# Kernel optimization log

Measured on AMD Instinct MI355X. Metric: run time of the kernel, lower is better.

The kernel has to match this reference:

```python
import jax, jax.numpy as jnp
import numpy as np

DIM = 1024
HEADS = 16
DIM_HEAD = 64
INNER = HEADS * DIM_HEAD  # 1024
P = INNER  # num_param_tokens
B, N = 4, 2048
LN_EPS = 1e-5
NORM_EPS = 1e-12


def _pattention(x, key_tok, val_tok):
    # x: [..., dim_in]; key_tok: [P, dim_in]; val_tok: [P, dim_out]
    scale = key_tok.shape[1] ** (-0.5)
    sim = jnp.einsum('bnd,pd->bnp', x, key_tok) * scale
    # F.normalize(p=2, dim=-1) with eps=1e-12
    nrm = jnp.maximum(jnp.linalg.norm(sim, axis=-1, keepdims=True), NORM_EPS)
    attn = jax.nn.gelu(sim / nrm, approximate=False)  # torch F.gelu default = exact erf
    return jnp.einsum('bnp,pe->bne', attn, val_tok)


def setup_inputs() -> dict:
    key = jax.random.key(0)
    ks = jax.random.split(key, 11)
    d = {
        'x': jax.random.normal(ks[0], (B, N, DIM), dtype=jnp.float32),
        'ln_gamma': jnp.ones((DIM,), dtype=jnp.float32),
        'ln_beta': jnp.zeros((DIM,), dtype=jnp.float32),
        'q_key': jax.random.normal(ks[1], (P, DIM), dtype=jnp.float32),
        'q_val': jax.random.normal(ks[2], (P, INNER), dtype=jnp.float32),
        'k_key': jax.random.normal(ks[3], (P, DIM), dtype=jnp.float32),
        'k_val': jax.random.normal(ks[4], (P, INNER), dtype=jnp.float32),
        'v_key': jax.random.normal(ks[5], (P, DIM), dtype=jnp.float32),
        'v_val': jax.random.normal(ks[6], (P, INNER), dtype=jnp.float32),
        'o_key': jax.random.normal(ks[7], (P, INNER), dtype=jnp.float32),
        'o_val': jax.random.normal(ks[8], (P, DIM), dtype=jnp.float32),
    }
    return d


def reference(x, ln_gamma, ln_beta, q_key, q_val, k_key, k_val, v_key, v_val, o_key, o_val):
    # LayerNorm (torch default: elementwise affine, eps=1e-5)
    mu = jnp.mean(x, axis=-1, keepdims=True)
    var = jnp.mean(jnp.square(x - mu), axis=-1, keepdims=True)
    x_norm = (x - mu) / jnp.sqrt(var + LN_EPS) * ln_gamma + ln_beta

    q = _pattention(x_norm, q_key, q_val)  # [B, N, INNER]
    k = _pattention(x_norm, k_key, k_val)
    v = _pattention(x_norm, v_key, v_val)

    # b n (h d) -> b h n d
    def split_heads(t):
        return t.reshape(B, N, HEADS, DIM_HEAD).transpose(0, 2, 1, 3)

    q, k, v = split_heads(q), split_heads(k), split_heads(v)
    scale = DIM_HEAD ** (-0.5)
    dots = jnp.einsum('bhnd,bhmd->bhnm', q, k) * scale  # [B, H, N, N]
    attn = jax.nn.softmax(dots, axis=-1)  # dropout p=0 -> identity
    out = jnp.einsum('bhnm,bhmd->bhnd', attn, v)
    out = out.transpose(0, 2, 1, 3).reshape(B, N, INNER)  # b h n d -> b n (h d)
    return _pattention(out, o_key, o_val)
```

## Files before the change

### kernel.cpp

```cpp
#include <hip/hip_runtime.h>
#include <hip/hip_bf16.h>
#include <stdint.h>

#define DIMSZ 1024
#define BN_TOT 8192
#define NSEQ 2048
#define NHEADS 16
#define DHEAD 64

typedef __attribute__((ext_vector_type(8))) __bf16 bf16x8;
typedef __attribute__((ext_vector_type(4))) float f32x4;

__device__ __forceinline__ float bf2f(ushort u) {
  return __uint_as_float(((uint32_t)u) << 16);
}
__device__ __forceinline__ ushort f2bf(float f) {
  uint32_t u = __float_as_uint(f);
  u += 0x7FFFu + ((u >> 16) & 1u);
  return (ushort)(u >> 16);
}
__device__ __forceinline__ uint32_t cvt_pk_bf16(float lo, float hi) {
  uint32_t r;
  asm("v_cvt_pk_bf16_f32 %0, %1, %2" : "=v"(r) : "v"(lo), "v"(hi));
  return r;
}

__global__ __launch_bounds__(256) void layernorm_k(
    const float* __restrict__ x, const float* __restrict__ gamma,
    const float* __restrict__ beta, ushort* __restrict__ xn) {
  const int row = blockIdx.x;
  const int tid = threadIdx.x;
  const float* xr = x + (size_t)row * DIMSZ;
  float4 v = *(const float4*)(xr + tid * 4);
  float s = v.x + v.y + v.z + v.w;
  float ss = v.x * v.x + v.y * v.y + v.z * v.z + v.w * v.w;
#pragma unroll
  for (int o = 1; o < 64; o <<= 1) { s += __shfl_xor(s, o); ss += __shfl_xor(ss, o); }
  __shared__ float red[2][4];
  const int wid = tid >> 6;
  if ((tid & 63) == 0) { red[0][wid] = s; red[1][wid] = ss; }
  __syncthreads();
  s = red[0][0] + red[0][1] + red[0][2] + red[0][3];
  ss = red[1][0] + red[1][1] + red[1][2] + red[1][3];
  const float mu = s * (1.0f / DIMSZ);
  const float var = ss * (1.0f / DIMSZ) - mu * mu;
  const float rstd = rsqrtf(var + 1e-5f);
  float4 g = *(const float4*)(gamma + tid * 4);
  float4 bb = *(const float4*)(beta + tid * 4);
  ushort4 o4;
  o4.x = f2bf((v.x - mu) * rstd * g.x + bb.x);
  o4.y = f2bf((v.y - mu) * rstd * g.y + bb.y);
  o4.z = f2bf((v.z - mu) * rstd * g.z + bb.z);
  o4.w = f2bf((v.w - mu) * rstd * g.w + bb.w);
  *(ushort4*)(xn + (size_t)row * DIMSZ + tid * 4) = o4;
}

__global__ __launch_bounds__(256) void normgelu_k(
    const float* __restrict__ sim, ushort* __restrict__ out) {
  const int row = blockIdx.x;
  const int tid = threadIdx.x;
  const float* sr = sim + (size_t)row * DIMSZ;
  float4 v = *(const float4*)(sr + tid * 4);
  float ss = v.x * v.x + v.y * v.y + v.z * v.z + v.w * v.w;
#pragma unroll
  for (int o = 1; o < 64; o <<= 1) ss += __shfl_xor(ss, o);
  __shared__ float red[4];
  if ((tid & 63) == 0) red[tid >> 6] = ss;
  __syncthreads();
  ss = red[0] + red[1] + red[2] + red[3];
  const float inv = 1.0f / fmaxf(sqrtf(ss), 1e-12f);
  ushort4 o4;
  float x0;
  x0 = v.x * inv; o4.x = f2bf(0.5f * x0 * (1.0f + erff(x0 * 0.70710678118654752f)));
  x0 = v.y * inv; o4.y = f2bf(0.5f * x0 * (1.0f + erff(x0 * 0.70710678118654752f)));
  x0 = v.z * inv; o4.z = f2bf(0.5f * x0 * (1.0f + erff(x0 * 0.70710678118654752f)));
  x0 = v.w * inv; o4.w = f2bf(0.5f * x0 * (1.0f + erff(x0 * 0.70710678118654752f)));
  *(ushort4*)(out + (size_t)row * DIMSZ + tid * 4) = o4;
}

__global__ void cvt_k(const float* __restrict__ in, ushort* __restrict__ out, int n) {
  int i = (blockIdx.x * 256 + threadIdx.x) * 4;
  if (i < n) {
    float4 v = *(const float4*)(in + i);
    ushort4 o;
    o.x = f2bf(v.x); o.y = f2bf(v.y); o.z = f2bf(v.z); o.w = f2bf(v.w);
    *(ushort4*)(out + i) = o;
  }
}

__global__ __launch_bounds__(256) void transpose_cvt_k(
    const float* __restrict__ in, ushort* __restrict__ out) {
  __shared__ float t[32][33];
  const int tx = threadIdx.x & 31;
  const int ty = threadIdx.x >> 5;
  const int bx = blockIdx.x * 32;
  const int by = blockIdx.y * 32;
#pragma unroll
  for (int i = 0; i < 32; i += 8)
    t[ty + i][tx] = in[(size_t)(by + ty + i) * DIMSZ + bx + tx];
  __syncthreads();
#pragma unroll
  for (int i = 0; i < 32; i += 8)
    out[(size_t)(bx + ty + i) * DIMSZ + by + tx] = f2bf(t[tx][ty + i]);
}

__global__ __launch_bounds__(256) void transpose_v_k(
    const ushort* __restrict__ vb, ushort* __restrict__ vt) {
  __shared__ ushort t[32][33];
  const int bh = blockIdx.x;
  const int nt = blockIdx.y;
  const int dt = blockIdx.z;
  const int b = bh >> 4, h = bh & 15;
  const int tx = threadIdx.x & 31;
  const int ty = threadIdx.x >> 5;
  const size_t inbase = ((size_t)b * NSEQ + nt * 32) * DIMSZ + h * DHEAD + dt * 32;
#pragma unroll
  for (int i = 0; i < 32; i += 8)
    t[ty + i][tx] = vb[inbase + (size_t)(ty + i) * DIMSZ + tx];
  __syncthreads();
  const size_t outbase = ((size_t)bh * DHEAD + dt * 32) * NSEQ + nt * 32;
#pragma unroll
  for (int i = 0; i < 32; i += 8)
    vt[outbase + (size_t)(ty + i) * NSEQ + tx] = t[tx][ty + i];
}

template <int OUT_BF16>
__global__ __launch_bounds__(256) void gemm_nt_k(
    const ushort* __restrict__ A, const ushort* __restrict__ B,
    void* __restrict__ Cout, int M, int N, int K) {
  __shared__ ushort As[128 * 40];
  __shared__ ushort Bs[128 * 40];
  const int tid = threadIdx.x;
  const int lane = tid & 63;
  const int wid = tid >> 6;
  const int i0 = blockIdx.x * 128;
  const int n0 = blockIdx.y * 128;
  const int wr = (wid >> 1) * 64;
  const int wc = (wid & 1) * 64;
  f32x4 acc[4][4];
#pragma unroll
  for (int m = 0; m < 4; ++m)
#pragma unroll
    for (int n = 0; n < 4; ++n) acc[m][n] = (f32x4){0.f, 0.f, 0.f, 0.f};
  const int srow = tid >> 2;
  const int skc = (tid & 3) * 8;
  const ushort* Ag = A + (size_t)i0 * K + skc;
  const ushort* Bg = B + (size_t)n0 * K + skc;
  const int fr = lane & 15;
  const int kg = (lane >> 4) * 8;
  uint4 a0 = *(const uint4*)(Ag + (size_t)srow * K);
  uint4 a1 = *(const uint4*)(Ag + (size_t)(srow + 64) * K);
  uint4 b0 = *(const uint4*)(Bg + (size_t)srow * K);
  uint4 b1 = *(const uint4*)(Bg + (size_t)(srow + 64) * K);
  for (int k0 = 0; k0 < K; k0 += 32) {
    __syncthreads();
    *(uint4*)&As[srow * 40 + skc] = a0;
    *(uint4*)&As[(srow + 64) * 40 + skc] = a1;
    *(uint4*)&Bs[srow * 40 + skc] = b0;
    *(uint4*)&Bs[(srow + 64) * 40 + skc] = b1;
    __syncthreads();
    if (k0 + 32 < K) {
      a0 = *(const uint4*)(Ag + (size_t)srow * K + k0 + 32);
      a1 = *(const uint4*)(Ag + (size_t)(srow + 64) * K + k0 + 32);
      b0 = *(const uint4*)(Bg + (size_t)srow * K + k0 + 32);
      b1 = *(const uint4*)(Bg + (size_t)(srow + 64) * K + k0 + 32);
    }
    bf16x8 af[4], bfr[4];
#pragma unroll
    for (int m = 0; m < 4; ++m)
      af[m] = *(const bf16x8*)&As[(wr + m * 16 + fr) * 40 + kg];
#pragma unroll
    for (int n = 0; n < 4; ++n)
      bfr[n] = *(const bf16x8*)&Bs[(wc + n * 16 + fr) * 40 + kg];
#pragma unroll
    for (int m = 0; m < 4; ++m)
#pragma unroll
      for (int n = 0; n < 4; ++n)
        acc[m][n] = __builtin_amdgcn_mfma_f32_16x16x32_bf16(af[m], bfr[n], acc[m][n], 0, 0, 0);
  }
  const int rq = lane >> 4;
#pragma unroll
  for (int m = 0; m < 4; ++m) {
#pragma unroll
    for (int n = 0; n < 4; ++n) {
#pragma unroll
      for (int rr = 0; rr < 4; ++rr) {
        const int row = i0 + wr + m * 16 + rq * 4 + rr;
        const int col = n0 + wc + n * 16 + fr;
        if (OUT_BF16)
          ((ushort*)Cout)[(size_t)row * N + col] = f2bf(acc[m][n][rr]);
        else
          ((float*)Cout)[(size_t)row * N + col] = acc[m][n][rr];
      }
    }
  }
}

__global__ __launch_bounds__(256) void flash_mfma_k(
    const ushort* __restrict__ Qm, const ushort* __restrict__ Km,
    const ushort* __restrict__ Vt, ushort* __restrict__ Om) {
  __shared__ ushort Ks[64 * 72];
  __shared__ ushort Vs[64 * 72];
  __shared__ ushort Ps[4][32 * 72];
  const int tid = threadIdx.x;
  const int lane = tid & 63;
  const int wid = tid >> 6;
  const int bh = blockIdx.x;
  const int qb = blockIdx.y;
  const int bidx = bh >> 4;
  const int h = bh & 15;
  const size_t rowbase = (size_t)bidx * NSEQ;
  const int colbase = h * DHEAD;
  const int fr = lane & 15;
  const int g = lane >> 4;
  const int kg = g * 8;
  const int q0 = qb * 128 + wid * 32;

  bf16x8 qf[2][2];
#pragma unroll
  for (int m = 0; m < 2; ++m)
#pragma unroll
    for (int ks = 0; ks < 2; ++ks)
      qf[m][ks] = *(const bf16x8*)(Qm + (rowbase + q0 + m * 16 + fr) * (size_t)DIMSZ +
                                   colbase + ks * 32 + kg);

  f32x4 oaccT[2][4];
#pragma unroll
  for (int m = 0; m < 2; ++m)
#pragma unroll
    for (int n = 0; n < 4; ++n) oaccT[m][n] = (f32x4){0.f, 0.f, 0.f, 0.f};
  float m2[2] = {-1e30f, -1e30f};
  float l_run[2] = {0.f, 0.f};
  const float c1 = 0.125f * 1.44269504088896340736f;

  const ushort* Kg = Km + rowbase * DIMSZ + colbase;
  const ushort* Vg = Vt + (size_t)bh * DHEAD * NSEQ;
  const int sr = tid >> 3;
  const int c8 = (tid & 7) * 8;

  uint4 k0 = *(const uint4*)(Kg + (size_t)sr * DIMSZ + c8);
  uint4 k1 = *(const uint4*)(Kg + (size_t)(sr + 32) * DIMSZ + c8);
  uint4 v0 = *(const uint4*)(Vg + (size_t)sr * NSEQ + c8);
  uint4 v1 = *(const uint4*)(Vg + (size_t)(sr + 32) * NSEQ + c8);

  for (int kt = 0; kt < NSEQ / 64; ++kt) {
    __syncthreads();
    *(uint4*)&Ks[sr * 72 + c8] = k0;
    *(uint4*)&Ks[(sr + 32) * 72 + c8] = k1;
    *(uint4*)&Vs[sr * 72 + c8] = v0;
    *(uint4*)&Vs[(sr + 32) * 72 + c8] = v1;
    __syncthreads();
    if (kt + 1 < NSEQ / 64) {
      k0 = *(const uint4*)(Kg + (size_t)((kt + 1) * 64 + sr) * DIMSZ + c8);
      k1 = *(const uint4*)(Kg + (size_t)((kt + 1) * 64 + sr + 32) * DIMSZ + c8);
      v0 = *(const uint4*)(Vg + (size_t)sr * NSEQ + (kt + 1) * 64 + c8);
      v1 = *(const uint4*)(Vg + (size_t)(sr + 32) * NSEQ + (kt + 1) * 64 + c8);
    }

    f32x4 s[2][4];
#pragma unroll
    for (int m = 0; m < 2; ++m)
#pragma unroll
      for (int n = 0; n < 4; ++n) s[m][n] = (f32x4){0.f, 0.f, 0.f, 0.f};
    __builtin_amdgcn_s_setprio(1);
#pragma unroll
    for (int ks = 0; ks < 2; ++ks) {
      bf16x8 ak[4];
#pragma unroll
      for (int n = 0; n < 4; ++n)
        ak[n] = *(const bf16x8*)&Ks[(n * 16 + fr) * 72 + ks * 32 + kg];
#pragma unroll
      for (int m = 0; m < 2; ++m)
#pragma unroll
        for (int n = 0; n < 4; ++n)
          s[m][n] = __builtin_amdgcn_mfma_f32_16x16x32_bf16(ak[n], qf[m][ks], s[m][n], 0, 0, 0);
    }
    __builtin_amdgcn_s_setprio(0);

#pragma unroll
    for (int m = 0; m < 2; ++m) {
      float tm = fmaxf(fmaxf(fmaxf(s[m][0][0], s[m][0][1]), fmaxf(s[m][0][2], s[m][0][3])),
                       fmaxf(fmaxf(s[m][1][0], s[m][1][1]), fmaxf(s[m][1][2], s[m][1][3])));
      tm = fmaxf(tm,
                 fmaxf(fmaxf(fmaxf(s[m][2][0], s[m][2][1]), fmaxf(s[m][2][2], s[m][2][3])),
                       fmaxf(fmaxf(s[m][3][0], s[m][3][1]), fmaxf(s[m][3][2], s[m][3][3]))));
      tm = fmaxf(tm, __shfl_xor(tm, 16));
      tm = fmaxf(tm, __shfl_xor(tm, 32));
      const float mn2 = fmaxf(m2[m], tm * c1);
      const float al = exp2f(m2[m] - mn2);
      float ps = 0.f;
#pragma unroll
      for (int n = 0; n < 4; ++n)
#pragma unroll
        for (int rr = 0; rr < 4; ++rr) {
          const float p = exp2f(fmaf(s[m][n][rr], c1, -mn2));
          s[m][n][rr] = p;
          ps += p;
        }
      ps += __shfl_xor(ps, 16);
      ps += __shfl_xor(ps, 32);
      l_run[m] = l_run[m] * al + ps;
      m2[m] = mn2;
#pragma unroll
      for (int n = 0; n < 4; ++n) oaccT[m][n] *= al;
    }

    ushort* pw = &Ps[wid][0];
#pragma unroll
    for (int m = 0; m < 2; ++m)
#pragma unroll
      for (int n = 0; n < 4; ++n) {
        uint2 w;
        w.x = cvt_pk_bf16(s[m][n][0], s[m][n][1]);
        w.y = cvt_pk_bf16(s[m][n][2], s[m][n][3]);
        *(uint2*)&pw[(m * 16 + fr) * 72 + n * 16 + g * 4] = w;
      }

    __builtin_amdgcn_s_setprio(1);
#pragma unroll
    for (int ks = 0; ks < 2; ++ks) {
      bf16x8 av[4], pb[2];
#pragma unroll
      for (int nd = 0; nd < 4; ++nd)
        av[nd] = *(const bf16x8*)&Vs[(nd * 16 + fr) * 72 + ks * 32 + kg];
#pragma unroll
      for (int m = 0; m < 2; ++m)
        pb[m] = *(const bf16x8*)&Ps[wid][(m * 16 + fr) * 72 + ks * 32 + kg];
#pragma unroll
      for (int m = 0; m < 2; ++m)
#pragma unroll
        for (int nd = 0; nd < 4; ++nd)
          oaccT[m][nd] = __builtin_amdgcn_mfma_f32_16x16x32_bf16(av[nd], pb[m], oaccT[m][nd], 0, 0, 0);
    }
    __builtin_amdgcn_s_setprio(0);
  }

#pragma unroll
  for (int m = 0; m < 2; ++m) {
    const float invl = 1.0f / l_run[m];
    const size_t row = rowbase + q0 + m * 16 + fr;
#pragma unroll
    for (int nd = 0; nd < 4; ++nd) {
      uint2 w;
      w.x = cvt_pk_bf16(oaccT[m][nd][0] * invl, oaccT[m][nd][1] * invl);
      w.y = cvt_pk_bf16(oaccT[m][nd][2] * invl, oaccT[m][nd][3] * invl);
      *(uint2*)(Om + row * DIMSZ + colbase + nd * 16 + g * 4) = w;
    }
  }
}

extern "C" void kernel_launch(void* const* d_in, const int* in_sizes, int n_in,
                              void* d_out, int out_size, void* d_ws, size_t ws_size,
                              hipStream_t stream) {
  (void)in_sizes; (void)n_in; (void)out_size; (void)ws_size;
  const float* x     = (const float*)d_in[0];
  const float* ln_g  = (const float*)d_in[1];
  const float* ln_b  = (const float*)d_in[2];
  const float* q_key = (const float*)d_in[3];
  const float* q_val = (const float*)d_in[4];
  const float* k_key = (const float*)d_in[5];
  const float* k_val = (const float*)d_in[6];
  const float* v_key = (const float*)d_in[7];
  const float* v_val = (const float*)d_in[8];
  const float* o_key = (const float*)d_in[9];
  const float* o_val = (const float*)d_in[10];
  float* out = (float*)d_out;

  char* ws = (char*)d_ws;
  const size_t MB = 1024 * 1024;
  ushort* xn    = (ushort*)(ws + 0 * MB);
  ushort* wkey  = (ushort*)(ws + 16 * MB);
  ushort* wvalT = (ushort*)(ws + 24 * MB);
  ushort* gelu  = (ushort*)(ws + 32 * MB);
  ushort* qb    = (ushort*)(ws + 48 * MB);
  ushort* kb    = (ushort*)(ws + 64 * MB);
  ushort* vb    = (ushort*)(ws + 80 * MB);
  ushort* aout  = (ushort*)(ws + 96 * MB);
  ushort* vt    = gelu;
  float* sim = (float*)d_out;

  const int NW = DIMSZ * DIMSZ;

  layernorm_k<<<BN_TOT, 256, 0, stream>>>(x, ln_g, ln_b, xn);
  cvt_k<<<1024, 256, 0, stream>>>(q_key, wkey + 0 * (size_t)NW, NW);
  cvt_k<<<1024, 256, 0, stream>>>(k_key, wkey + 1 * (size_t)NW, NW);
  cvt_k<<<1024, 256, 0, stream>>>(v_key, wkey + 2 * (size_t)NW, NW);
  cvt_k<<<1024, 256, 0, stream>>>(o_key, wkey + 3 * (size_t)NW, NW);
  dim3 tg(32, 32);
  transpose_cvt_k<<<tg, 256, 0, stream>>>(q_val, wvalT + 0 * (size_t)NW);
  transpose_cvt_k<<<tg, 256, 0, stream>>>(k_val, wvalT + 1 * (size_t)NW);
  transpose_cvt_k<<<tg, 256, 0, stream>>>(v_val, wvalT + 2 * (size_t)NW);
  transpose_cvt_k<<<tg, 256, 0, stream>>>(o_val, wvalT + 3 * (size_t)NW);

  dim3 gg(BN_TOT / 128, DIMSZ / 128);
  ushort* outs[3] = {qb, kb, vb};
  for (int t = 0; t < 3; ++t) {
    gemm_nt_k<0><<<gg, 256, 0, stream>>>(xn, wkey + t * (size_t)NW, sim, BN_TOT, DIMSZ, DIMSZ);
    normgelu_k<<<BN_TOT, 256, 0, stream>>>(sim, gelu);
    gemm_nt_k<1><<<gg, 256, 0, stream>>>(gelu, wvalT + t * (size_t)NW, outs[t], BN_TOT, DIMSZ, DIMSZ);
  }
  transpose_v_k<<<dim3(64, 64, 2), 256, 0, stream>>>(vb, vt);
  flash_mfma_k<<<dim3(64, 16), 256, 0, stream>>>(qb, kb, vt, aout);
  gemm_nt_k<0><<<gg, 256, 0, stream>>>(aout, wkey + 3 * (size_t)NW, sim, BN_TOT, DIMSZ, DIMSZ);
  normgelu_k<<<BN_TOT, 256, 0, stream>>>(sim, gelu);
  gemm_nt_k<0><<<gg, 256, 0, stream>>>(gelu, wvalT + 3 * (size_t)NW, (void*)out, BN_TOT, DIMSZ, DIMSZ);
}
```

Measured before the change: 451.1 us.

## Use direct global-to-LDS loads in GEMM, lazy softmax rescale, occupancy hint

The GEMM now loads tiles with global_load_lds straight into unpadded LDS, replacing the register-staged prefetch. This drops VGPR staging but loses the overlap of the next tile's load with compute and can add bank conflicts because the padding is gone. The flash-attention kernel gets a launch-bounds occupancy hint of 4 blocks. Its online softmax now rescales the running max only when the new max exceeds the old one by more than 8 in log2 units, and sums the row with a tree reduction. This skips many rescale multiplies and exps at the cost of some extra numeric range.

New measurement: 452.4 us. No clear change (+0.3%).

```diff
diff --git a/kernel.cpp b/kernel.cpp
--- a/kernel.cpp
+++ b/kernel.cpp
@@ -23,6 +23,11 @@
   uint32_t r;
   asm("v_cvt_pk_bf16_f32 %0, %1, %2" : "=v"(r) : "v"(lo), "v"(hi));
   return r;
+}
+__device__ __forceinline__ void gl_lds16(const ushort* g, ushort* l) {
+  __builtin_amdgcn_global_load_lds(
+      (const __attribute__((address_space(1))) void*)g,
+      (__attribute__((address_space(3))) void*)l, 16, 0, 0);
 }
 
 __global__ __launch_bounds__(256) void layernorm_k(
@@ -128,8 +133,8 @@
 __global__ __launch_bounds__(256) void gemm_nt_k(
     const ushort* __restrict__ A, const ushort* __restrict__ B,
     void* __restrict__ Cout, int M, int N, int K) {
-  __shared__ ushort As[128 * 40];
-  __shared__ ushort Bs[128 * 40];
+  __shared__ ushort As[128 * 32];
+  __shared__ ushort Bs[128 * 32];
   const int tid = threadIdx.x;
   const int lane = tid & 63;
   const int wid = tid >> 6;
@@ -142,36 +147,28 @@
   for (int m = 0; m < 4; ++m)
 #pragma unroll
     for (int n = 0; n < 4; ++n) acc[m][n] = (f32x4){0.f, 0.f, 0.f, 0.f};
-  const int srow = tid >> 2;
-  const int skc = (tid & 3) * 8;
-  const ushort* Ag = A + (size_t)i0 * K + skc;
-  const ushort* Bg = B + (size_t)n0 * K + skc;
   const int fr = lane & 15;
   const int kg = (lane >> 4) * 8;
-  uint4 a0 = *(const uint4*)(Ag + (size_t)srow * K);
-  uint4 a1 = *(const uint4*)(Ag + (size_t)(srow + 64) * K);
-  uint4 b0 = *(const uint4*)(Bg + (size_t)srow * K);
-  uint4 b1 = *(const uint4*)(Bg + (size_t)(srow + 64) * K);
+  const int srow = wid * 32 + (lane >> 2);
+  const int skc = (lane & 3) * 8;
+  const ushort* Ag = A + (size_t)(i0 + srow) * K + skc;
+  const ushort* Bg = B + (size_t)(n0 + srow) * K + skc;
+  ushort* AsW = As + wid * 1024;
+  ushort* BsW = Bs + wid * 1024;
   for (int k0 = 0; k0 < K; k0 += 32) {
     __syncthreads();
-    *(uint4*)&As[srow * 40 + skc] = a0;
-    *(uint4*)&As[(srow + 64) * 40 + skc] = a1;
-    *(uint4*)&Bs[srow * 40 + skc] = b0;
-    *(uint4*)&Bs[(srow + 64) * 40 + skc] = b1;
+    gl_lds16(Ag + k0, AsW);
+    gl_lds16(Ag + (size_t)16 * K + k0, AsW + 512);
+    gl_lds16(Bg + k0, BsW);
+    gl_lds16(Bg + (size_t)16 * K + k0, BsW + 512);
     __syncthreads();
-    if (k0 + 32 < K) {
-      a0 = *(const uint4*)(Ag + (size_t)srow * K + k0 + 32);
-      a1 = *(const uint4*)(Ag + (size_t)(srow + 64) * K + k0 + 32);
-      b0 = *(const uint4*)(Bg + (size_t)srow * K + k0 + 32);
-      b1 = *(const uint4*)(Bg + (size_t)(srow + 64) * K + k0 + 32);
-    }
     bf16x8 af[4], bfr[4];
 #pragma unroll
     for (int m = 0; m < 4; ++m)
-      af[m] = *(const bf16x8*)&As[(wr + m * 16 + fr) * 40 + kg];
+      af[m] = *(const bf16x8*)&As[(wr + m * 16 + fr) * 32 + kg];
 #pragma unroll
     for (int n = 0; n < 4; ++n)
-      bfr[n] = *(const bf16x8*)&Bs[(wc + n * 16 + fr) * 40 + kg];
+      bfr[n] = *(const bf16x8*)&Bs[(wc + n * 16 + fr) * 32 + kg];
 #pragma unroll
     for (int m = 0; m < 4; ++m)
 #pragma unroll
@@ -196,7 +193,7 @@
   }
 }
 
-__global__ __launch_bounds__(256) void flash_mfma_k(
+__global__ __launch_bounds__(256, 4) void flash_mfma_k(
     const ushort* __restrict__ Qm, const ushort* __restrict__ Km,
     const ushort* __restrict__ Vt, ushort* __restrict__ Om) {
   __shared__ ushort Ks[64 * 72];
@@ -286,23 +283,32 @@
                        fmaxf(fmaxf(s[m][3][0], s[m][3][1]), fmaxf(s[m][3][2], s[m][3][3]))));
       tm = fmaxf(tm, __shfl_xor(tm, 16));
       tm = fmaxf(tm, __shfl_xor(tm, 32));
-      const float mn2 = fmaxf(m2[m], tm * c1);
-      const float al = exp2f(m2[m] - mn2);
-      float ps = 0.f;
+      const float tm2 = tm * c1;
+      if (!__all(tm2 <= m2[m] + 8.0f)) {
+        const float mn2 = fmaxf(m2[m], tm2);
+        const float al = exp2f(m2[m] - mn2);
+        l_run[m] *= al;
+        m2[m] = mn2;
+#pragma unroll
+        for (int n = 0; n < 4; ++n) oaccT[m][n] *= al;
+      }
+      const float mref = m2[m];
+      float p[4][4];
 #pragma unroll
       for (int n = 0; n < 4; ++n)
 #pragma unroll
         for (int rr = 0; rr < 4; ++rr) {
-          const float p = exp2f(fmaf(s[m][n][rr], c1, -mn2));
-          s[m][n][rr] = p;
-          ps += p;
+          p[n][rr] = exp2f(fmaf(s[m][n][rr], c1, -mref));
+          s[m][n][rr] = p[n][rr];
         }
+      const float t0 = (p[0][0] + p[0][1]) + (p[0][2] + p[0][3]);
+      const float t1 = (p[1][0] + p[1][1]) + (p[1][2] + p[1][3]);
+      const float t2 = (p[2][0] + p[2][1]) + (p[2][2] + p[2][3]);
+      const float t3 = (p[3][0] + p[3][1]) + (p[3][2] + p[3][3]);
+      float ps = (t0 + t1) + (t2 + t3);
       ps += __shfl_xor(ps, 16);
       ps += __shfl_xor(ps, 32);
-      l_run[m] = l_run[m] * al + ps;
-      m2[m] = mn2;
-#pragma unroll
-      for (int n = 0; n < 4; ++n) oaccT[m][n] *= al;
+      l_run[m] += ps;
     }
 
     ushort* pw = &Ps[wid][0];
```
